# Performance work log

Measured on AMD Instinct MI355X. Metric: run time of the kernel, lower is better.

## Reference

```python
import jax, jax.numpy as jnp
import numpy as np

BATCH, D, N = 16, 128, 16
E = N * (N - 1) // 2  # 120 candidate edges (strict upper triangle)


def _incidence(A, n):
    """Build edge-incidence matrices G, H of shape [b, n, E] from binary edge
    vector A [b, E] over the strict upper triangle of an n x n adjacency."""
    r, c = np.triu_indices(n, k=1)
    mask = (A > 0).astype(jnp.float32)  # [b, E]
    node = jnp.arange(n)[:, None]       # [n, 1]
    G = (node == jnp.asarray(r)[None, :]).astype(jnp.float32)[None] * mask[:, None, :]
    H = (node == jnp.asarray(c)[None, :]).astype(jnp.float32)[None] * mask[:, None, :]
    return G, H


def _kron(t1, t2):
    """Batched Kronecker product: t1 [b,r1,c1], t2 [b,r2,c2] -> [b,r1*r2,c1*c2]."""
    b, r1, c1 = t1.shape
    _, r2, c2 = t2.shape
    return (t1[:, :, None, :, None] * t2[:, None, :, None, :]).reshape(b, r1 * r2, c1 * c2)


def setup_inputs() -> dict:
    key = jax.random.key(0)
    ks = jax.random.split(key, 8)
    A_src = jax.random.randint(ks[0], (BATCH, E), 0, 2, dtype=jnp.int32)
    A_tgt = jax.random.randint(ks[1], (BATCH, E), 0, 2, dtype=jnp.int32)
    F_src = jax.random.normal(ks[2], (BATCH, D, N), dtype=jnp.float32)
    F_tgt = jax.random.normal(ks[3], (BATCH, D, N), dtype=jnp.float32)
    U_src = jax.random.normal(ks[4], (BATCH, N, N), dtype=jnp.float32)
    U_tgt = jax.random.normal(ks[5], (BATCH, N, N), dtype=jnp.float32)
    stdv = 1.0 / np.sqrt(D * 2)
    eye_half = jnp.eye(D, dtype=jnp.float32) / 2.0
    lambda1 = jax.random.uniform(ks[6], (D, D), jnp.float32, -stdv, stdv) + eye_half
    lambda2 = jax.random.uniform(ks[7], (D, D), jnp.float32, -stdv, stdv) + eye_half
    return {"A_src": A_src, "A_tgt": A_tgt, "F_src": F_src, "F_tgt": F_tgt,
            "U_src": U_src, "U_tgt": U_tgt, "lambda1": lambda1, "lambda2": lambda2}


def reference(A_src, A_tgt, F_src, F_tgt, U_src, U_tgt, lambda1, lambda2):
    b = F_src.shape[0]
    n, m = F_src.shape[-1], F_tgt.shape[-1]
    # symmetrized, relu'd block weight (w1 = w2 = 1)
    l1 = jax.nn.relu(lambda1 + lambda1.T)
    l2 = jax.nn.relu(lambda2 + lambda2.T)
    weight = jnp.block([[l1, l2], [l2, l1]])  # [2d, 2d]
    # incidence matrices (vectorized replacement of the per-batch scatter loop)
    G1, H1 = _incidence(A_src, n)  # [b, n, E]
    G2, H2 = _incidence(A_tgt, m)  # [b, m, E]
    # edge features: X = cat(F G, F H) -> [b, 2d, E]
    X = jnp.concatenate([F_src @ G1, F_src @ H1], axis=1)
    Y = jnp.concatenate([F_tgt @ G2, F_tgt @ H2], axis=1)
    # edge affinity M_e = X^T W Y : [b, E, E]
    M_e = jnp.einsum('bie,ij,bjf->bef', X, weight, Y)
    # node affinity M_p = U_src^T U_tgt : [b, n, m]
    M_p = jnp.einsum('bdn,bdm->bnm', U_src, U_tgt)
    K1 = _kron(G2, G1)  # [b, m*n, E*E]
    K2 = _kron(H2, H1)  # [b, m*n, E*E]
    # per-column scaling of K1 by flattened M_e (replaces per-column loop)
    K1_new = K1 * M_e.reshape(b, 1, -1)
    diagMp = jax.vmap(jnp.diag)(M_p.reshape(b, -1))  # [b, n*m, n*m]
    M = diagMp + jnp.einsum('bik,bjk->bij', K1_new, K2)
    return M
```

## Files before the change

kernel.cpp:

```cpp
#include <hip/hip_runtime.h>


#define LS 132
#define TS 17
#define CH 32

__device__ __forceinline__ int edge_idx(int a, int p) {
    return (a * (31 - a)) / 2 + (p - a - 1);
}

__global__ __launch_bounds__(256) void kOne(
    const int* __restrict__ Asrc, const int* __restrict__ Atgt,
    const float* __restrict__ Fsrc, const float* __restrict__ Ftgt,
    const float* __restrict__ Usrc, const float* __restrict__ Utgt,
    const float* __restrict__ lam1, const float* __restrict__ lam2,
    float* __restrict__ out)
{
    __shared__ float sRow1[CH * LS], sCol1[CH * LS];
    __shared__ float sRow2[CH * LS], sCol2[CH * LS];
    __shared__ float sW1[CH * LS], sW2[CH * LS];
    __shared__ float sFsT[16 * LS];
    __shared__ float sFtT[16 * LS];
    __shared__ float sS1[16 * LS], sS2[16 * LS];
    __shared__ float sU[512];
    __shared__ float sP1[16 * TS], sP2[16 * TS], sMp[256];
    __shared__ int   smask[120];

    const int blk = blockIdx.x;
    const int b   = blk >> 4;
    const int a   = blk & 15;
    const int t   = threadIdx.x;

    {
        const float4* fsp = (const float4*)(Fsrc + b * 2048);
        const float4* ftp = (const float4*)(Ftgt + b * 2048);
#pragma unroll
        for (int it = 0; it < 2; ++it) {
            const int k = t + it * 256;
            const int d = k >> 2, x0 = (k & 3) * 4;
            const float4 f = fsp[k];
            sFsT[(x0 + 0) * LS + d] = f.x;
            sFsT[(x0 + 1) * LS + d] = f.y;
            sFsT[(x0 + 2) * LS + d] = f.z;
            sFsT[(x0 + 3) * LS + d] = f.w;
            const float4 g = ftp[k];
            sFtT[(x0 + 0) * LS + d] = g.x;
            sFtT[(x0 + 1) * LS + d] = g.y;
            sFtT[(x0 + 2) * LS + d] = g.z;
            sFtT[(x0 + 3) * LS + d] = g.w;
        }
        if (t < 64)       ((float4*)sU)[t] = ((const float4*)(Usrc + b * 256))[t];
        else if (t < 128) ((float4*)sU)[t] = ((const float4*)(Utgt + b * 256))[t - 64];
        if (t < 120) smask[t] = (Asrc[b * 120 + t] > 0) && (Atgt[b * 120 + t] > 0);
    }

    const int u  = t >> 4;
    const int jg = t & 15;
    float acc1[8], acc2[8];
#pragma unroll
    for (int s = 0; s < 8; ++s) { acc1[s] = 0.f; acc2[s] = 0.f; }

    for (int i0 = 0; i0 < 128; i0 += CH) {
        const float4* r1 = (const float4*)(lam1 + i0 * 128);
        const float4* r2 = (const float4*)(lam2 + i0 * 128);
#pragma unroll
        for (int it = 0; it < 4; ++it) {
            const int k = t + it * 256;
            const int il = k >> 5, j4 = k & 31;
            *(float4*)(&sRow1[il * LS + j4 * 4]) = r1[il * 32 + j4];
            *(float4*)(&sRow2[il * LS + j4 * 4]) = r2[il * 32 + j4];
        }
#pragma unroll
        for (int it = 0; it < 16; ++it) {
            const int k = t + it * 256;
            const int il = k & 31, j = k >> 5;
            sCol1[il * LS + j] = lam1[j * 128 + i0 + il];
            sCol2[il * LS + j] = lam2[j * 128 + i0 + il];
        }
        __syncthreads();

#pragma unroll
        for (int g = 0; g < 4; ++g) {
            const int k = t + g * 256;
            const int il = k >> 5, j4 = (k & 31) * 4;
            const float4 r = *(const float4*)(&sRow1[il * LS + j4]);
            const float4 c = *(const float4*)(&sCol1[il * LS + j4]);
            float4 w;
            w.x = fmaxf(r.x + c.x, 0.f);  w.y = fmaxf(r.y + c.y, 0.f);
            w.z = fmaxf(r.z + c.z, 0.f);  w.w = fmaxf(r.w + c.w, 0.f);
            *(float4*)(&sW1[il * LS + j4]) = w;
            const float4 r2v = *(const float4*)(&sRow2[il * LS + j4]);
            const float4 c2v = *(const float4*)(&sCol2[il * LS + j4]);
            float4 w2;
            w2.x = fmaxf(r2v.x + c2v.x, 0.f);  w2.y = fmaxf(r2v.y + c2v.y, 0.f);
            w2.z = fmaxf(r2v.z + c2v.z, 0.f);  w2.w = fmaxf(r2v.w + c2v.w, 0.f);
            *(float4*)(&sW2[il * LS + j4]) = w2;
        }
        __syncthreads();

#pragma unroll 8
        for (int il = 0; il < CH; ++il) {
            const float f1 = sFsT[u * LS + i0 + il];
            const float4 wA = *(const float4*)(&sW1[il * LS + jg * 4]);
            const float4 wB = *(const float4*)(&sW1[il * LS + 64 + jg * 4]);
            acc1[0] = fmaf(f1, wA.x, acc1[0]);  acc1[1] = fmaf(f1, wA.y, acc1[1]);
            acc1[2] = fmaf(f1, wA.z, acc1[2]);  acc1[3] = fmaf(f1, wA.w, acc1[3]);
            acc1[4] = fmaf(f1, wB.x, acc1[4]);  acc1[5] = fmaf(f1, wB.y, acc1[5]);
            acc1[6] = fmaf(f1, wB.z, acc1[6]);  acc1[7] = fmaf(f1, wB.w, acc1[7]);
            const float4 vA = *(const float4*)(&sW2[il * LS + jg * 4]);
            const float4 vB = *(const float4*)(&sW2[il * LS + 64 + jg * 4]);
            acc2[0] = fmaf(f1, vA.x, acc2[0]);  acc2[1] = fmaf(f1, vA.y, acc2[1]);
            acc2[2] = fmaf(f1, vA.z, acc2[2]);  acc2[3] = fmaf(f1, vA.w, acc2[3]);
            acc2[4] = fmaf(f1, vB.x, acc2[4]);  acc2[5] = fmaf(f1, vB.y, acc2[5]);
            acc2[6] = fmaf(f1, vB.z, acc2[6]);  acc2[7] = fmaf(f1, vB.w, acc2[7]);
        }
        __syncthreads();
    }

    *(float4*)(&sS1[u * LS + jg * 4])      = make_float4(acc1[0], acc1[1], acc1[2], acc1[3]);
    *(float4*)(&sS1[u * LS + 64 + jg * 4]) = make_float4(acc1[4], acc1[5], acc1[6], acc1[7]);
    *(float4*)(&sS2[u * LS + jg * 4])      = make_float4(acc2[0], acc2[1], acc2[2], acc2[3]);
    *(float4*)(&sS2[u * LS + 64 + jg * 4]) = make_float4(acc2[4], acc2[5], acc2[6], acc2[7]);
    __syncthreads();

    {
        const int u2 = t >> 4, v = t & 15;
        float p1 = 0.f, p2 = 0.f;
#pragma unroll 8
        for (int j0 = 0; j0 < 128; j0 += 4) {
            const float4 ft = *(const float4*)(&sFtT[v * LS + j0]);
            const float4 s1 = *(const float4*)(&sS1[u2 * LS + j0]);
            const float4 s2 = *(const float4*)(&sS2[u2 * LS + j0]);
            p1 = fmaf(s1.x, ft.x, p1);  p2 = fmaf(s2.x, ft.x, p2);
            p1 = fmaf(s1.y, ft.y, p1);  p2 = fmaf(s2.y, ft.y, p2);
            p1 = fmaf(s1.z, ft.z, p1);  p2 = fmaf(s2.z, ft.z, p2);
            p1 = fmaf(s1.w, ft.w, p1);  p2 = fmaf(s2.w, ft.w, p2);
        }
        float mp = 0.f;
#pragma unroll
        for (int d = 0; d < 16; ++d)
            mp = fmaf(sU[(d << 4) | u2], sU[256 + ((d << 4) | v)], mp);
        sP1[u2 * TS + v] = p1;
        sP2[u2 * TS + v] = p2;
        sMp[t] = mp;
    }
    __syncthreads();

    const int j0c = (t & 63) << 2;
    const int p   = j0c >> 4;
    const bool condA = (a < p) && (smask[edge_idx(a, p)] != 0);
    float* outR = out + ((size_t)b << 16) + (a << 12);
#pragma unroll
    for (int rr = 0; rr < 4; ++rr) {
        const int c = (t >> 6) + (rr << 2);
        const int r = (a << 4) | c;
        const float cpart = sP1[a * TS + c] + sP2[p * TS + c];
        float4 vec;
        float* vv = (float*)&vec;
#pragma unroll
        for (int s = 0; s < 4; ++s) {
            const int j = j0c + s, q = j & 15;
            float x = 0.f;
            if (condA && (c < q) && (smask[edge_idx(c, q)] != 0))
                x = cpart + sP2[a * TS + q] + sP1[p * TS + q];
            if (r == j) x += sMp[r];
            vv[s] = x;
        }
        *(float4*)(outR + (c << 8) + j0c) = vec;
    }
}

extern "C" void kernel_launch(void* const* d_in, const int* in_sizes, int n_in,
                              void* d_out, int out_size, void* d_ws, size_t ws_size,
                              hipStream_t stream) {
    const int*   A_src = (const int*)d_in[0];
    const int*   A_tgt = (const int*)d_in[1];
    const float* F_src = (const float*)d_in[2];
    const float* F_tgt = (const float*)d_in[3];
    const float* U_src = (const float*)d_in[4];
    const float* U_tgt = (const float*)d_in[5];
    const float* lam1  = (const float*)d_in[6];
    const float* lam2  = (const float*)d_in[7];
    float* out = (float*)d_out;

    kOne<<<256, 256, 0, stream>>>(A_src, A_tgt, F_src, F_tgt,
                                  U_src, U_tgt, lam1, lam2, out);
}
```

Measured before the change: 85.63 us.

## Restructure weight GEMM into 4x4 register tiles with in-place symmetrization and larger chunks

Replaces the separate row/column staging buffers for lambda with a single buffer per lambda: the transposed slice is written first, then the row slice is added in place with relu, halving the shared memory used for weight staging. The F_src·W product now gives each thread a 4x4 register tile, with half the threads on lambda1 and half on lambda2. Each thread reads one float4 of F and one float4 of W per step instead of a scalar plus four float4s. The chunk size doubles to 64, so there are fewer loop iterations and barriers. The transposed global load of lambda uses strided float4 reads that are not coalesced, and the block's shared memory footprint changes, which may affect occupancy.

After: 85.10 us. Within noise of the previous version (-0.6%).

```diff
diff --git a/kernel.cpp b/kernel.cpp
--- a/kernel.cpp
+++ b/kernel.cpp
@@ -3,7 +3,7 @@
 
 #define LS 132
 #define TS 17
-#define CH 32
+#define CH 64
 
 __device__ __forceinline__ int edge_idx(int a, int p) {
     return (a * (31 - a)) / 2 + (p - a - 1);
@@ -16,12 +16,10 @@
     const float* __restrict__ lam1, const float* __restrict__ lam2,
     float* __restrict__ out)
 {
-    __shared__ float sRow1[CH * LS], sCol1[CH * LS];
-    __shared__ float sRow2[CH * LS], sCol2[CH * LS];
-    __shared__ float sW1[CH * LS], sW2[CH * LS];
-    __shared__ float sFsT[16 * LS];
+    __shared__ float sW[2][CH * LS];
+    __shared__ float sFs[2048];
     __shared__ float sFtT[16 * LS];
-    __shared__ float sS1[16 * LS], sS2[16 * LS];
+    __shared__ float sS[2][16 * LS];
     __shared__ float sU[512];
     __shared__ float sP1[16 * TS], sP2[16 * TS], sMp[256];
     __shared__ int   smask[120];
@@ -37,90 +35,91 @@
 #pragma unroll
         for (int it = 0; it < 2; ++it) {
             const int k = t + it * 256;
-            const int d = k >> 2, x0 = (k & 3) * 4;
-            const float4 f = fsp[k];
-            sFsT[(x0 + 0) * LS + d] = f.x;
-            sFsT[(x0 + 1) * LS + d] = f.y;
-            sFsT[(x0 + 2) * LS + d] = f.z;
-            sFsT[(x0 + 3) * LS + d] = f.w;
+            ((float4*)sFs)[k] = fsp[k];
+            const int d = k >> 2, v0 = (k & 3) * 4;
             const float4 g = ftp[k];
-            sFtT[(x0 + 0) * LS + d] = g.x;
-            sFtT[(x0 + 1) * LS + d] = g.y;
-            sFtT[(x0 + 2) * LS + d] = g.z;
-            sFtT[(x0 + 3) * LS + d] = g.w;
+            sFtT[(v0 + 0) * LS + d] = g.x;
+            sFtT[(v0 + 1) * LS + d] = g.y;
+            sFtT[(v0 + 2) * LS + d] = g.z;
+            sFtT[(v0 + 3) * LS + d] = g.w;
         }
         if (t < 64)       ((float4*)sU)[t] = ((const float4*)(Usrc + b * 256))[t];
         else if (t < 128) ((float4*)sU)[t] = ((const float4*)(Utgt + b * 256))[t - 64];
         if (t < 120) smask[t] = (Asrc[b * 120 + t] > 0) && (Atgt[b * 120 + t] > 0);
     }
 
-    const int u  = t >> 4;
-    const int jg = t & 15;
-    float acc1[8], acc2[8];
+    const int lsel = t >> 7;
+    const int tl   = t & 127;
+    const int ug   = tl >> 5;
+    const int jg   = tl & 31;
+    const float* lamG[2] = { lam1, lam2 };
+    float acc[4][4];
 #pragma unroll
-    for (int s = 0; s < 8; ++s) { acc1[s] = 0.f; acc2[s] = 0.f; }
+    for (int r = 0; r < 4; ++r)
+#pragma unroll
+        for (int s = 0; s < 4; ++s) acc[r][s] = 0.f;
 
     for (int i0 = 0; i0 < 128; i0 += CH) {
-        const float4* r1 = (const float4*)(lam1 + i0 * 128);
-        const float4* r2 = (const float4*)(lam2 + i0 * 128);
-#pragma unroll
-        for (int it = 0; it < 4; ++it) {
-            const int k = t + it * 256;
-            const int il = k >> 5, j4 = k & 31;
-            *(float4*)(&sRow1[il * LS + j4 * 4]) = r1[il * 32 + j4];
-            *(float4*)(&sRow2[il * LS + j4 * 4]) = r2[il * 32 + j4];
-        }
 #pragma unroll
         for (int it = 0; it < 16; ++it) {
-            const int k = t + it * 256;
-            const int il = k & 31, j = k >> 5;
-            sCol1[il * LS + j] = lam1[j * 128 + i0 + il];
-            sCol2[il * LS + j] = lam2[j * 128 + i0 + il];
+            const int k  = t + it * 256;
+            const int l  = k >> 11;
+            const int kk = k & 2047;
+            const int j  = kk & 127, g = kk >> 7;
+            const float4 f = ((const float4*)lamG[l])[j * 32 + (i0 >> 2) + g];
+            sW[l][(4 * g + 0) * LS + j] = f.x;
+            sW[l][(4 * g + 1) * LS + j] = f.y;
+            sW[l][(4 * g + 2) * LS + j] = f.z;
+            sW[l][(4 * g + 3) * LS + j] = f.w;
         }
         __syncthreads();
 
 #pragma unroll
-        for (int g = 0; g < 4; ++g) {
-            const int k = t + g * 256;
-            const int il = k >> 5, j4 = (k & 31) * 4;
-            const float4 r = *(const float4*)(&sRow1[il * LS + j4]);
-            const float4 c = *(const float4*)(&sCol1[il * LS + j4]);
-            float4 w;
-            w.x = fmaxf(r.x + c.x, 0.f);  w.y = fmaxf(r.y + c.y, 0.f);
-            w.z = fmaxf(r.z + c.z, 0.f);  w.w = fmaxf(r.w + c.w, 0.f);
-            *(float4*)(&sW1[il * LS + j4]) = w;
-            const float4 r2v = *(const float4*)(&sRow2[il * LS + j4]);
-            const float4 c2v = *(const float4*)(&sCol2[il * LS + j4]);
-            float4 w2;
-            w2.x = fmaxf(r2v.x + c2v.x, 0.f);  w2.y = fmaxf(r2v.y + c2v.y, 0.f);
-            w2.z = fmaxf(r2v.z + c2v.z, 0.f);  w2.w = fmaxf(r2v.w + c2v.w, 0.f);
-            *(float4*)(&sW2[il * LS + j4]) = w2;
+        for (int it = 0; it < 16; ++it) {
+            const int k  = t + it * 256;
+            const int l  = k >> 11;
+            const int kk = k & 2047;
+            const int il = kk >> 5, jb = kk & 31;
+            const float4 row = ((const float4*)lamG[l])[(i0 + il) * 32 + jb];
+            float* wp = &sW[l][il * LS + 4 * jb];
+            float4 w = *(float4*)wp;
+            w.x = fmaxf(w.x + row.x, 0.f);
+            w.y = fmaxf(w.y + row.y, 0.f);
+            w.z = fmaxf(w.z + row.z, 0.f);
+            w.w = fmaxf(w.w + row.w, 0.f);
+            *(float4*)wp = w;
         }
         __syncthreads();
 
+        const float* sWl = sW[lsel];
 #pragma unroll 8
         for (int il = 0; il < CH; ++il) {
-            const float f1 = sFsT[u * LS + i0 + il];
-            const float4 wA = *(const float4*)(&sW1[il * LS + jg * 4]);
-            const float4 wB = *(const float4*)(&sW1[il * LS + 64 + jg * 4]);
-            acc1[0] = fmaf(f1, wA.x, acc1[0]);  acc1[1] = fmaf(f1, wA.y, acc1[1]);
-            acc1[2] = fmaf(f1, wA.z, acc1[2]);  acc1[3] = fmaf(f1, wA.w, acc1[3]);
-            acc1[4] = fmaf(f1, wB.x, acc1[4]);  acc1[5] = fmaf(f1, wB.y, acc1[5]);
-            acc1[6] = fmaf(f1, wB.z, acc1[6]);  acc1[7] = fmaf(f1, wB.w, acc1[7]);
-            const float4 vA = *(const float4*)(&sW2[il * LS + jg * 4]);
-            const float4 vB = *(const float4*)(&sW2[il * LS + 64 + jg * 4]);
-            acc2[0] = fmaf(f1, vA.x, acc2[0]);  acc2[1] = fmaf(f1, vA.y, acc2[1]);
-            acc2[2] = fmaf(f1, vA.z, acc2[2]);  acc2[3] = fmaf(f1, vA.w, acc2[3]);
-            acc2[4] = fmaf(f1, vB.x, acc2[4]);  acc2[5] = fmaf(f1, vB.y, acc2[5]);
-            acc2[6] = fmaf(f1, vB.z, acc2[6]);  acc2[7] = fmaf(f1, vB.w, acc2[7]);
+            const float4 fs = *(const float4*)(&sFs[(i0 + il) * 16 + 4 * ug]);
+            const float4 w  = *(const float4*)(&sWl[il * LS + 4 * jg]);
+            acc[0][0] = fmaf(fs.x, w.x, acc[0][0]);
+            acc[0][1] = fmaf(fs.x, w.y, acc[0][1]);
+            acc[0][2] = fmaf(fs.x, w.z, acc[0][2]);
+            acc[0][3] = fmaf(fs.x, w.w, acc[0][3]);
+            acc[1][0] = fmaf(fs.y, w.x, acc[1][0]);
+            acc[1][1] = fmaf(fs.y, w.y, acc[1][1]);
+            acc[1][2] = fmaf(fs.y, w.z, acc[1][2]);
+            acc[1][3] = fmaf(fs.y, w.w, acc[1][3]);
+            acc[2][0] = fmaf(fs.z, w.x, acc[2][0]);
+            acc[2][1] = fmaf(fs.z, w.y, acc[2][1]);
+            acc[2][2] = fmaf(fs.z, w.z, acc[2][2]);
+            acc[2][3] = fmaf(fs.z, w.w, acc[2][3]);
+            acc[3][0] = fmaf(fs.w, w.x, acc[3][0]);
+            acc[3][1] = fmaf(fs.w, w.y, acc[3][1]);
+            acc[3][2] = fmaf(fs.w, w.z, acc[3][2]);
+            acc[3][3] = fmaf(fs.w, w.w, acc[3][3]);
         }
         __syncthreads();
     }
 
-    *(float4*)(&sS1[u * LS + jg * 4])      = make_float4(acc1[0], acc1[1], acc1[2], acc1[3]);
-    *(float4*)(&sS1[u * LS + 64 + jg * 4]) = make_float4(acc1[4], acc1[5], acc1[6], acc1[7]);
-    *(float4*)(&sS2[u * LS + jg * 4])      = make_float4(acc2[0], acc2[1], acc2[2], acc2[3]);
-    *(float4*)(&sS2[u * LS + 64 + jg * 4]) = make_float4(acc2[4], acc2[5], acc2[6], acc2[7]);
+#pragma unroll
+    for (int r = 0; r < 4; ++r)
+        *(float4*)(&sS[lsel][(4 * ug + r) * LS + 4 * jg]) =
+            make_float4(acc[r][0], acc[r][1], acc[r][2], acc[r][3]);
     __syncthreads();
 
     {
@@ -129,8 +128,8 @@
 #pragma unroll 8
         for (int j0 = 0; j0 < 128; j0 += 4) {
             const float4 ft = *(const float4*)(&sFtT[v * LS + j0]);
-            const float4 s1 = *(const float4*)(&sS1[u2 * LS + j0]);
-            const float4 s2 = *(const float4*)(&sS2[u2 * LS + j0]);
+            const float4 s1 = *(const float4*)(&sS[0][u2 * LS + j0]);
+            const float4 s2 = *(const float4*)(&sS[1][u2 * LS + j0]);
             p1 = fmaf(s1.x, ft.x, p1);  p2 = fmaf(s2.x, ft.x, p2);
             p1 = fmaf(s1.y, ft.y, p1);  p2 = fmaf(s2.y, ft.y, p2);
             p1 = fmaf(s1.z, ft.z, p1);  p2 = fmaf(s2.z, ft.z, p2);
```
